# Kernel optimization log

Hardware: AMD Instinct MI355X
Metric: run time of the kernel (lower is better)

## Reference

```python
import jax, jax.numpy as jnp
import numpy as np

NUM_CAPSULE = 5
DIM_CAPSULE = 5
ROUTINGS = 4
T_EPSILON = 1e-07


def squash(x, axis=-1):
    # Note: this module's 'squash' is pure norm-normalization (no v^2/(1+v^2) factor)
    s_squared_norm = jnp.sum(x * x, axis=axis, keepdims=True)
    return x / jnp.sqrt(s_squared_norm + T_EPSILON)


def setup_inputs() -> dict:
    key = jax.random.key(0)
    k1, k2 = jax.random.split(key)
    batch, seq, d_in = 1024, 512, 120
    x = jax.random.normal(k1, (batch, seq, d_in), dtype=jnp.float32)
    # xavier_normal for fan_in=120, fan_out=25
    std = float(np.sqrt(2.0 / (d_in + NUM_CAPSULE * DIM_CAPSULE)))
    W = jax.random.normal(k2, (1, d_in, NUM_CAPSULE * DIM_CAPSULE), dtype=jnp.float32) * std
    return {"x": x, "W": W}


def reference(x, W):
    batch, inp, _ = x.shape
    # u_hat_vecs: [batch, num_capsule, input_num_capsule, dim_capsule]
    u_hat = jnp.matmul(x, W[0])  # [b, inp, 25]
    u_hat = u_hat.reshape(batch, inp, NUM_CAPSULE, DIM_CAPSULE).transpose(0, 2, 1, 3)
    b = jnp.zeros((batch, NUM_CAPSULE, inp), dtype=u_hat.dtype)
    outputs = None
    for i in range(ROUTINGS):
        # torch code softmaxes over the num_capsule axis (dim 1 of b)
        c = jax.nn.softmax(b, axis=1)  # [b, ncaps, inp]
        outputs = squash(jnp.einsum('bij,bijk->bik', c, u_hat))  # [b, ncaps, dcap]
        if i < ROUTINGS - 1:
            b = jnp.einsum('bik,bijk->bij', outputs, u_hat)
    return outputs
```

## Files before the change

kernel.cpp:

```cpp
#include <hip/hip_runtime.h>


#define NCAP 5
#define DCAP 5
#define NOUT 25
#define DIN 120
#define SEQ 512
#define ROUTINGS 4

#define KT   24
#define PAD  26

__global__ __launch_bounds__(256) void caps_kernel(
    const float* __restrict__ x,
    const float* __restrict__ W,
    float* __restrict__ out)
{
    const int b    = blockIdx.x;
    const int t    = threadIdx.x;
    const int lane = t & 63;
    const int wv   = t >> 6;

    __shared__ float xt[SEQ * PAD];
    __shared__ float red[4][NOUT];

    const float* xb = x + (size_t)b * SEQ * DIN;

    float acc[2][NOUT];
#pragma unroll
    for (int r = 0; r < 2; ++r)
#pragma unroll
        for (int j = 0; j < NOUT; ++j) acc[r][j] = 0.f;

    const int r0 = (2 * t) * PAD;
    const int r1 = (2 * t + 1) * PAD;

    for (int tile = 0; tile < 5; ++tile) {
        const int k0 = tile * KT;

#pragma unroll
        for (int i = 0; i < 12; ++i) {
            int f   = t + 256 * i;
            int row = f / 6;
            int q   = f - row * 6;
            float4 v = *(const float4*)(xb + row * DIN + k0 + 4 * q);
            float* dst = &xt[row * PAD + 4 * q];
            *(float2*)(dst)     = make_float2(v.x, v.y);
            *(float2*)(dst + 2) = make_float2(v.z, v.w);
        }
        __syncthreads();

#pragma unroll
        for (int u = 0; u < 6; ++u) {
            float2 a0 = *(const float2*)&xt[r0 + 4 * u];
            float2 a1 = *(const float2*)&xt[r0 + 4 * u + 2];
            float2 b0 = *(const float2*)&xt[r1 + 4 * u];
            float2 b1 = *(const float2*)&xt[r1 + 4 * u + 2];
            const float* wr = W + (k0 + 4 * u) * NOUT;
#pragma unroll
            for (int j = 0; j < NOUT; ++j) {
                float w0 = wr[j];
                float w1 = wr[j + NOUT];
                float w2 = wr[j + 2 * NOUT];
                float w3 = wr[j + 3 * NOUT];
                acc[0][j] = fmaf(a1.y, w3, fmaf(a1.x, w2, fmaf(a0.y, w1, fmaf(a0.x, w0, acc[0][j]))));
                acc[1][j] = fmaf(b1.y, w3, fmaf(b1.x, w2, fmaf(b0.y, w1, fmaf(b0.x, w0, acc[1][j]))));
            }
        }
        __syncthreads();
    }

    float bb[2][NCAP];
#pragma unroll
    for (int r = 0; r < 2; ++r)
#pragma unroll
        for (int c = 0; c < NCAP; ++c) bb[r][c] = 0.f;

    float o[NOUT];

    for (int it = 0; it < ROUTINGS; ++it) {
        float p[NOUT];
#pragma unroll
        for (int j = 0; j < NOUT; ++j) p[j] = 0.f;

#pragma unroll
        for (int r = 0; r < 2; ++r) {
            float m = bb[r][0];
#pragma unroll
            for (int c = 1; c < NCAP; ++c) m = fmaxf(m, bb[r][c]);
            float e[NCAP]; float se = 0.f;
#pragma unroll
            for (int c = 0; c < NCAP; ++c) { e[c] = __expf(bb[r][c] - m); se += e[c]; }
            float inv = 1.f / se;
#pragma unroll
            for (int c = 0; c < NCAP; ++c) {
                float cc = e[c] * inv;
#pragma unroll
                for (int k = 0; k < DCAP; ++k)
                    p[c*DCAP + k] = fmaf(cc, acc[r][c*DCAP + k], p[c*DCAP + k]);
            }
        }

#pragma unroll
        for (int d = 1; d < 64; d <<= 1)
#pragma unroll
            for (int j = 0; j < NOUT; ++j) p[j] += __shfl_xor(p[j], d, 64);

        if (lane == 0) {
#pragma unroll
            for (int j = 0; j < NOUT; ++j) red[wv][j] = p[j];
        }
        __syncthreads();
        float s[NOUT];
#pragma unroll
        for (int j = 0; j < NOUT; ++j)
            s[j] = red[0][j] + red[1][j] + red[2][j] + red[3][j];
        __syncthreads();

#pragma unroll
        for (int c = 0; c < NCAP; ++c) {
            float ss = 0.f;
#pragma unroll
            for (int k = 0; k < DCAP; ++k)
                ss = fmaf(s[c*DCAP + k], s[c*DCAP + k], ss);
            float sc = rsqrtf(ss + 1e-7f);
#pragma unroll
            for (int k = 0; k < DCAP; ++k) o[c*DCAP + k] = s[c*DCAP + k] * sc;
        }

        if (it < ROUTINGS - 1) {
#pragma unroll
            for (int r = 0; r < 2; ++r)
#pragma unroll
                for (int c = 0; c < NCAP; ++c) {
                    float d0 = 0.f;
#pragma unroll
                    for (int k = 0; k < DCAP; ++k)
                        d0 = fmaf(o[c*DCAP + k], acc[r][c*DCAP + k], d0);
                    bb[r][c] = d0;
                }
        }
    }

    if (t < NOUT) out[(size_t)b * NOUT + t] = o[t];
}

extern "C" void kernel_launch(void* const* d_in, const int* in_sizes, int n_in,
                              void* d_out, int out_size, void* d_ws, size_t ws_size,
                              hipStream_t stream) {
    const float* x   = (const float*)d_in[0];
    const float* W   = (const float*)d_in[1];
    float*       o   = (float*)d_out;
    const int batch  = in_sizes[0] / (SEQ * DIN);
    caps_kernel<<<dim3(batch), dim3(256), 0, stream>>>(x, W, o);
}
```

Baseline: 402.6 us.

## Transpose LDS tile to k-major with odd row stride and halve K tile

The x tile in shared memory is now stored k-major with a row stride of 513 floats, so each thread reads its sequence row as a conflict-free scalar per k instead of float2 reads from padded rows. The K tile shrinks from 24 to 12, which cuts LDS use to about 24.6 KB, and launch bounds request 5 blocks per CU to raise occupancy. The costs are scalar transposing stores into LDS, which may bank-conflict, and twice as many tile iterations and barriers.

```diff
diff --git a/kernel.cpp b/kernel.cpp
--- a/kernel.cpp
+++ b/kernel.cpp
@@ -8,10 +8,10 @@
 #define SEQ 512
 #define ROUTINGS 4
 
-#define KT   24
-#define PAD  26
+#define KT    12
+#define LROW  513
 
-__global__ __launch_bounds__(256) void caps_kernel(
+__global__ __launch_bounds__(256, 5) void caps_kernel(
     const float* __restrict__ x,
     const float* __restrict__ W,
     float* __restrict__ out)
@@ -21,7 +21,7 @@
     const int lane = t & 63;
     const int wv   = t >> 6;
 
-    __shared__ float xt[SEQ * PAD];
+    __shared__ float xt[KT * LROW];
     __shared__ float red[4][NOUT];
 
     const float* xb = x + (size_t)b * SEQ * DIN;
@@ -32,39 +32,32 @@
 #pragma unroll
         for (int j = 0; j < NOUT; ++j) acc[r][j] = 0.f;
 
-    const int r0 = (2 * t) * PAD;
-    const int r1 = (2 * t + 1) * PAD;
-
-    for (int tile = 0; tile < 5; ++tile) {
+    for (int tile = 0; tile < 10; ++tile) {
         const int k0 = tile * KT;
 
 #pragma unroll
-        for (int i = 0; i < 12; ++i) {
+        for (int i = 0; i < 6; ++i) {
             int f   = t + 256 * i;
-            int row = f / 6;
-            int q   = f - row * 6;
+            int row = f / 3;
+            int q   = f - row * 3;
             float4 v = *(const float4*)(xb + row * DIN + k0 + 4 * q);
-            float* dst = &xt[row * PAD + 4 * q];
-            *(float2*)(dst)     = make_float2(v.x, v.y);
-            *(float2*)(dst + 2) = make_float2(v.z, v.w);
+            xt[(4 * q + 0) * LROW + row] = v.x;
+            xt[(4 * q + 1) * LROW + row] = v.y;
+            xt[(4 * q + 2) * LROW + row] = v.z;
+            xt[(4 * q + 3) * LROW + row] = v.w;
         }
         __syncthreads();
 
 #pragma unroll
-        for (int u = 0; u < 6; ++u) {
-            float2 a0 = *(const float2*)&xt[r0 + 4 * u];
-            float2 a1 = *(const float2*)&xt[r0 + 4 * u + 2];
-            float2 b0 = *(const float2*)&xt[r1 + 4 * u];
-            float2 b1 = *(const float2*)&xt[r1 + 4 * u + 2];
-            const float* wr = W + (k0 + 4 * u) * NOUT;
+        for (int k = 0; k < KT; ++k) {
+            float a  = xt[k * LROW + t];
+            float bv = xt[k * LROW + t + 256];
+            const float* wr = W + (k0 + k) * NOUT;
 #pragma unroll
             for (int j = 0; j < NOUT; ++j) {
-                float w0 = wr[j];
-                float w1 = wr[j + NOUT];
-                float w2 = wr[j + 2 * NOUT];
-                float w3 = wr[j + 3 * NOUT];
-                acc[0][j] = fmaf(a1.y, w3, fmaf(a1.x, w2, fmaf(a0.y, w1, fmaf(a0.x, w0, acc[0][j]))));
-                acc[1][j] = fmaf(b1.y, w3, fmaf(b1.x, w2, fmaf(b0.y, w1, fmaf(b0.x, w0, acc[1][j]))));
+                float w = wr[j];
+                acc[0][j] = fmaf(a,  w, acc[0][j]);
+                acc[1][j] = fmaf(bv, w, acc[1][j]);
             }
         }
         __syncthreads();
```

New measurement: 473.2 us. +17.5%, slower.

## Load each row directly into registers, drop LDS staging, one row per thread

Applied to the files above, without the earlier changes.

Each of 512 threads now loads its full 120-float input row into registers as float4 vectors and computes the 25 projections without shared-memory tiling or block barriers. Routing state shrinks to one row per thread, and the cross-wave reduction grows to 8 waves. This removes LDS traffic and the sync stalls of the tiled loop. In exchange it raises register pressure and uses strided per-lane global loads that coalesce less well.

```diff
diff --git a/kernel.cpp b/kernel.cpp
--- a/kernel.cpp
+++ b/kernel.cpp
@@ -7,11 +7,9 @@
 #define DIN 120
 #define SEQ 512
 #define ROUTINGS 4
+#define NQ   30
 
-#define KT   24
-#define PAD  26
-
-__global__ __launch_bounds__(256) void caps_kernel(
+__global__ __launch_bounds__(512) void caps_kernel(
     const float* __restrict__ x,
     const float* __restrict__ W,
     float* __restrict__ out)
@@ -21,84 +19,57 @@
     const int lane = t & 63;
     const int wv   = t >> 6;
 
-    __shared__ float xt[SEQ * PAD];
-    __shared__ float red[4][NOUT];
+    __shared__ float red[8][NOUT];
 
-    const float* xb = x + (size_t)b * SEQ * DIN;
+    const float* xr = x + (size_t)b * SEQ * DIN + (size_t)t * DIN;
 
-    float acc[2][NOUT];
+    float4 rv[NQ];
 #pragma unroll
-    for (int r = 0; r < 2; ++r)
+    for (int q = 0; q < NQ; ++q)
+        rv[q] = *(const float4*)(xr + 4 * q);
+
+    float acc[NOUT];
 #pragma unroll
-        for (int j = 0; j < NOUT; ++j) acc[r][j] = 0.f;
-
-    const int r0 = (2 * t) * PAD;
-    const int r1 = (2 * t + 1) * PAD;
-
-    for (int tile = 0; tile < 5; ++tile) {
-        const int k0 = tile * KT;
+    for (int j = 0; j < NOUT; ++j) acc[j] = 0.f;
 
 #pragma unroll
-        for (int i = 0; i < 12; ++i) {
-            int f   = t + 256 * i;
-            int row = f / 6;
-            int q   = f - row * 6;
-            float4 v = *(const float4*)(xb + row * DIN + k0 + 4 * q);
-            float* dst = &xt[row * PAD + 4 * q];
-            *(float2*)(dst)     = make_float2(v.x, v.y);
-            *(float2*)(dst + 2) = make_float2(v.z, v.w);
+    for (int q = 0; q < NQ; ++q) {
+        const float* wr = W + (4 * q) * NOUT;
+#pragma unroll
+        for (int j = 0; j < NOUT; ++j) {
+            float w0 = wr[j];
+            float w1 = wr[j + NOUT];
+            float w2 = wr[j + 2 * NOUT];
+            float w3 = wr[j + 3 * NOUT];
+            acc[j] = fmaf(rv[q].w, w3,
+                     fmaf(rv[q].z, w2,
+                     fmaf(rv[q].y, w1,
+                     fmaf(rv[q].x, w0, acc[j]))));
         }
-        __syncthreads();
-
-#pragma unroll
-        for (int u = 0; u < 6; ++u) {
-            float2 a0 = *(const float2*)&xt[r0 + 4 * u];
-            float2 a1 = *(const float2*)&xt[r0 + 4 * u + 2];
-            float2 b0 = *(const float2*)&xt[r1 + 4 * u];
-            float2 b1 = *(const float2*)&xt[r1 + 4 * u + 2];
-            const float* wr = W + (k0 + 4 * u) * NOUT;
-#pragma unroll
-            for (int j = 0; j < NOUT; ++j) {
-                float w0 = wr[j];
-                float w1 = wr[j + NOUT];
-                float w2 = wr[j + 2 * NOUT];
-                float w3 = wr[j + 3 * NOUT];
-                acc[0][j] = fmaf(a1.y, w3, fmaf(a1.x, w2, fmaf(a0.y, w1, fmaf(a0.x, w0, acc[0][j]))));
-                acc[1][j] = fmaf(b1.y, w3, fmaf(b1.x, w2, fmaf(b0.y, w1, fmaf(b0.x, w0, acc[1][j]))));
-            }
-        }
-        __syncthreads();
     }
 
-    float bb[2][NCAP];
+    float bb[NCAP];
 #pragma unroll
-    for (int r = 0; r < 2; ++r)
-#pragma unroll
-        for (int c = 0; c < NCAP; ++c) bb[r][c] = 0.f;
+    for (int c = 0; c < NCAP; ++c) bb[c] = 0.f;
 
     float o[NOUT];
 
     for (int it = 0; it < ROUTINGS; ++it) {
+        float m = bb[0];
+#pragma unroll
+        for (int c = 1; c < NCAP; ++c) m = fmaxf(m, bb[c]);
+        float e[NCAP]; float se = 0.f;
+#pragma unroll
+        for (int c = 0; c < NCAP; ++c) { e[c] = __expf(bb[c] - m); se += e[c]; }
+        float inv = 1.f / se;
+
         float p[NOUT];
 #pragma unroll
-        for (int j = 0; j < NOUT; ++j) p[j] = 0.f;
-
+        for (int c = 0; c < NCAP; ++c) {
+            float cc = e[c] * inv;
 #pragma unroll
-        for (int r = 0; r < 2; ++r) {
-            float m = bb[r][0];
-#pragma unroll
-            for (int c = 1; c < NCAP; ++c) m = fmaxf(m, bb[r][c]);
-            float e[NCAP]; float se = 0.f;
-#pragma unroll
-            for (int c = 0; c < NCAP; ++c) { e[c] = __expf(bb[r][c] - m); se += e[c]; }
-            float inv = 1.f / se;
-#pragma unroll
-            for (int c = 0; c < NCAP; ++c) {
-                float cc = e[c] * inv;
-#pragma unroll
-                for (int k = 0; k < DCAP; ++k)
-                    p[c*DCAP + k] = fmaf(cc, acc[r][c*DCAP + k], p[c*DCAP + k]);
-            }
+            for (int k = 0; k < DCAP; ++k)
+                p[c*DCAP + k] = cc * acc[c*DCAP + k];
         }
 
 #pragma unroll
@@ -114,7 +85,8 @@
         float s[NOUT];
 #pragma unroll
         for (int j = 0; j < NOUT; ++j)
-            s[j] = red[0][j] + red[1][j] + red[2][j] + red[3][j];
+            s[j] = red[0][j] + red[1][j] + red[2][j] + red[3][j]
+                 + red[4][j] + red[5][j] + red[6][j] + red[7][j];
         __syncthreads();
 
 #pragma unroll
@@ -130,15 +102,13 @@
 
         if (it < ROUTINGS - 1) {
 #pragma unroll
-            for (int r = 0; r < 2; ++r)
+            for (int c = 0; c < NCAP; ++c) {
+                float d0 = 0.f;
 #pragma unroll
-                for (int c = 0; c < NCAP; ++c) {
-                    float d0 = 0.f;
-#pragma unroll
-                    for (int k = 0; k < DCAP; ++k)
-                        d0 = fmaf(o[c*DCAP + k], acc[r][c*DCAP + k], d0);
-                    bb[r][c] = d0;
-                }
+                for (int k = 0; k < DCAP; ++k)
+                    d0 = fmaf(o[c*DCAP + k], acc[c*DCAP + k], d0);
+                bb[c] = d0;
+            }
         }
     }
 
@@ -152,5 +122,5 @@
     const float* W   = (const float*)d_in[1];
     float*       o   = (float*)d_out;
     const int batch  = in_sizes[0] / (SEQ * DIN);
-    caps_kernel<<<dim3(batch), dim3(256), 0, stream>>>(x, W, o);
+    caps_kernel<<<dim3(batch), dim3(512), 0, stream>>>(x, W, o);
 }
```

Measured after the change: 486.3 us. 20.8% more time.
